# Performance work log

Hardware: AMD Instinct MI355X
Metric: run time of the kernel (lower is better)

Reference implementation:

```python
import jax, jax.numpy as jnp
import numpy as np

D_MODEL, D_Q, D_K, D_V, N = 1024, 128, 128, 128, 8192

def setup_inputs() -> dict:
    key = jax.random.key(0)
    ks = jax.random.split(key, 7)
    s = 1.0 / np.sqrt(D_MODEL)
    return {
        "x": jax.random.normal(ks[0], (N, D_MODEL), dtype=jnp.float32),
        "Wq": jax.random.uniform(ks[1], (D_MODEL, D_Q), jnp.float32, -s, s),
        "bq": jax.random.uniform(ks[2], (D_Q,), jnp.float32, -s, s),
        "Wk": jax.random.uniform(ks[3], (D_MODEL, D_K), jnp.float32, -s, s),
        "bk": jax.random.uniform(ks[4], (D_K,), jnp.float32, -s, s),
        "Wv": jax.random.uniform(ks[5], (D_MODEL, D_V), jnp.float32, -s, s),
        "bv": jax.random.uniform(ks[6], (D_V,), jnp.float32, -s, s),
    }

def reference(x, Wq, bq, Wk, bk, Wv, bv):
    q = x @ Wq + bq          # [N, d_q]
    k = x @ Wk + bk          # [N, d_k]
    v = x @ Wv + bv          # [N, d_v]
    scale = jnp.sqrt(jnp.asarray(q.shape[-1], q.dtype))
    scores = (q @ k.T) / scale          # [N, N]
    attn = jax.nn.softmax(scores, axis=1)  # matches nn.Softmax(dim=1) on 2D
    return attn @ v                     # [N, d_v]
```

## Files before the change

kernel.cpp:

```cpp
#include <hip/hip_runtime.h>


typedef __attribute__((ext_vector_type(8))) short bf16x8;
typedef __attribute__((ext_vector_type(4))) float f32x4;

#define NTOK 8192
#define DMODEL 1024
#define DH 128
#define NSPLIT 8
#define CPS 16

__device__ __forceinline__ unsigned short f2bf(float f) {
  unsigned int u = __builtin_bit_cast(unsigned int, f);
  u += 0x7fffu + ((u >> 16) & 1u);
  return (unsigned short)(u >> 16);
}

__device__ __forceinline__ unsigned int pack2bf(float a, float b) {
  return (unsigned int)f2bf(a) | ((unsigned int)f2bf(b) << 16);
}

__device__ __forceinline__ void gl2lds16(const void* gp, void* lp) {
  const __attribute__((address_space(1))) unsigned int* g =
      (const __attribute__((address_space(1))) unsigned int*)gp;
  __attribute__((address_space(3))) unsigned int* l =
      (__attribute__((address_space(3))) unsigned int*)lp;
  __builtin_amdgcn_global_load_lds(g, l, 16, 0, 0);
}

__global__ __launch_bounds__(256) void k_build_wt(const float* __restrict__ Wq,
                                                  const float* __restrict__ Wk,
                                                  const float* __restrict__ Wv,
                                                  unsigned short* __restrict__ wt) {
  __shared__ unsigned short tile[32 * 130];
  int k0 = blockIdx.x * 32;
  int p = blockIdx.y;
  int t = threadIdx.x;
  const float* W = (p == 0) ? Wq : ((p == 1) ? Wk : Wv);
  float vscale = (p == 2) ? 0.0625f : 1.0f;
#pragma unroll
  for (int i = 0; i < 16; i++) {
    int e = i * 256 + t;
    int n = e & 127, kk = e >> 7;
    tile[kk * 130 + n] = f2bf(W[(size_t)(k0 + kk) * DH + n] * vscale);
  }
  __syncthreads();
#pragma unroll
  for (int i = 0; i < 16; i++) {
    int e = i * 256 + t;
    int kk = e & 31, n = e >> 5;
    wt[(size_t)(p * DH + n) * DMODEL + k0 + kk] = tile[kk * 130 + n];
  }
}

__global__ __launch_bounds__(256, 2) void k_qkv(const float* __restrict__ x,
                                                const unsigned short* __restrict__ wt,
                                                const float* __restrict__ bq,
                                                const float* __restrict__ bk,
                                                const float* __restrict__ bv,
                                                unsigned short* __restrict__ qs,
                                                unsigned short* __restrict__ kkv,
                                                unsigned short* __restrict__ vt) {
  __shared__ float xt[2][64 * 64];
  __shared__ unsigned short wtt[2][128 * 64];
  int mt = blockIdx.x, p = blockIdx.y;
  int tid = threadIdx.x;
  int w = tid >> 6, lane = tid & 63, l16 = lane & 15, g = lane >> 4;

#define STAGE_QKV(buf, k0)                                                     \
  {                                                                            \
    _Pragma("unroll") for (int r = 0; r < 4; r++) {                            \
      int seg = r * 4 + w;                                                     \
      int xr = seg * 4 + (lane >> 4);                                          \
      int xlc = ((lane & 15) ^ (xr & 15)) & 15;                                \
      gl2lds16(&x[(size_t)(mt * 64 + xr) * DMODEL + (k0) + xlc * 4],           \
               &xt[buf][seg * 256]);                                           \
      int wc = seg * 8 + (lane >> 3);                                          \
      int wlc = ((lane & 7) ^ (wc & 7)) & 7;                                   \
      gl2lds16(&wt[(size_t)(p * DH + wc) * DMODEL + (k0) + wlc * 8],           \
               &wtt[buf][seg * 512]);                                          \
    }                                                                          \
  }

  f32x4 zero = {0.f, 0.f, 0.f, 0.f};
  f32x4 acc[8];
#pragma unroll
  for (int i = 0; i < 8; i++) acc[i] = zero;

  STAGE_QKV(0, 0);
  STAGE_QKV(1, 64);
  int arow = w * 16 + l16;
  for (int kt2 = 0; kt2 < 16; kt2++) {
    int b = kt2 & 1;
    if (kt2 < 15)
      asm volatile("s_waitcnt vmcnt(8)\n\ts_barrier" ::: "memory");
    else
      asm volatile("s_waitcnt vmcnt(0)\n\ts_barrier" ::: "memory");
    __builtin_amdgcn_sched_barrier(0);

    bf16x8 a[2];
#pragma unroll
    for (int half = 0; half < 2; half++) {
      int lc0 = half * 8 + g * 2;
      const f32x4 u0 = *(const f32x4*)&xt[b][arow * 64 + ((lc0 ^ l16) & 15) * 4];
      const f32x4 u1 = *(const f32x4*)&xt[b][arow * 64 + (((lc0 + 1) ^ l16) & 15) * 4];
      union { unsigned int u[4]; bf16x8 v; } pk;
      pk.u[0] = pack2bf(u0[0], u0[1]);
      pk.u[1] = pack2bf(u0[2], u0[3]);
      pk.u[2] = pack2bf(u1[0], u1[1]);
      pk.u[3] = pack2bf(u1[2], u1[3]);
      a[half] = pk.v;
    }
#pragma unroll
    for (int nt = 0; nt < 8; nt++) {
      int col = nt * 16 + l16;
#pragma unroll
      for (int half = 0; half < 2; half++) {
        int lc = half * 4 + g;
        bf16x8 bf = *(const bf16x8*)&wtt[b][col * 64 + ((lc ^ (col & 7)) & 7) * 8];
        acc[nt] = __builtin_amdgcn_mfma_f32_16x16x32_bf16(a[half], bf, acc[nt], 0, 0, 0);
      }
    }

    asm volatile("s_waitcnt lgkmcnt(0)\n\ts_barrier" ::: "memory");
    if (kt2 + 2 < 16) STAGE_QKV(b, (kt2 + 2) * 64);
  }
#undef STAGE_QKV

  const float* bias = (p == 0) ? bq : ((p == 1) ? bk : bv);
  float mult = (p == 0) ? (0.08838834764831845f * 1.44269504088896340f) : 1.0f;
  if (p < 2) {
    unsigned short* outp = (p == 0) ? qs : kkv;
#pragma unroll
    for (int nt = 0; nt < 8; nt++) {
      int col = nt * 16 + l16;
      float bsv = bias[col];
#pragma unroll
      for (int r = 0; r < 4; r++) {
        int row = mt * 64 + w * 16 + g * 4 + r;
        outp[(size_t)row * DH + col] = f2bf((acc[nt][r] + bsv) * mult);
      }
    }
  } else {
#pragma unroll
    for (int nt = 0; nt < 8; nt++) {
      int col = nt * 16 + l16;
      float bsv = bias[col] * 0.0625f;
      int row0 = mt * 64 + w * 16 + g * 4;
      uint2 uv;
      uv.x = pack2bf(acc[nt][0] + bsv, acc[nt][1] + bsv);
      uv.y = pack2bf(acc[nt][2] + bsv, acc[nt][3] + bsv);
      *(uint2*)(&vt[(size_t)col * NTOK + row0]) = uv;
    }
  }
}

__global__ __launch_bounds__(256, 2) void k_flash(const unsigned short* __restrict__ qs,
                                                  const unsigned short* __restrict__ kkv,
                                                  const unsigned short* __restrict__ vt,
                                                  _Float16* __restrict__ opart,
                                                  float* __restrict__ lpart) {
  __shared__ unsigned short kt[2][64 * 128];
  __shared__ unsigned short vtl[2][128 * 64];
  __shared__ unsigned short pscr[4 * 2 * 1024];
  int sp = blockIdx.x, qt = blockIdx.y;
  int tid = threadIdx.x;
  int w = tid >> 6, lane = tid & 63, l16 = lane & 15, g = lane >> 4;
  int swz2 = (l16 & 7) ^ ((l16 >> 3) << 1);

  bf16x8 qf[2][4];
  int qbase = qt * 128 + w * 32;
#pragma unroll
  for (int q2 = 0; q2 < 2; q2++)
#pragma unroll
    for (int f = 0; f < 4; f++)
      qf[q2][f] = *(const bf16x8*)(&qs[(size_t)(qbase + q2 * 16 + l16) * DH + f * 32 + g * 8]);

  int pcK[4], pcV[2], pcP[2];
#pragma unroll
  for (int f = 0; f < 4; f++) {
    int lc = f * 4 + g;
    pcK[f] = (lc & 8) | ((lc ^ l16) & 7);
  }
#pragma unroll
  for (int kb = 0; kb < 2; kb++) {
    int lc = kb * 4 + g;
    pcV[kb] = (lc ^ l16) & 7;
    pcP[kb] = (lc ^ swz2) & 7;
  }

#define STAGE_FLASH(buf, chunk)                                                 \
  {                                                                             \
    int key0 = (chunk) * 64;                                                    \
    _Pragma("unroll") for (int ii = 0; ii < 4; ii++) {                          \
      int i = w * 4 + ii;                                                       \
      int krow = 4 * i + (lane >> 4);                                           \
      int klc = ((lane & 15) & 8) | (((lane & 15) ^ krow) & 7);                 \
      gl2lds16(&kkv[(size_t)(key0 + krow) * DH + klc * 8], &kt[buf][i * 512]);  \
      int vrow = 8 * i + (lane >> 3);                                           \
      int vlc = ((lane & 7) ^ vrow) & 7;                                        \
      gl2lds16(&vt[(size_t)vrow * NTOK + key0 + vlc * 8], &vtl[buf][i * 512]);  \
    }                                                                           \
  }

  f32x4 zero = {0.f, 0.f, 0.f, 0.f};
  f32x4 o[2][8];
#pragma unroll
  for (int q2 = 0; q2 < 2; q2++)
#pragma unroll
    for (int dt = 0; dt < 8; dt++) o[q2][dt] = zero;
  float l[2] = {0.f, 0.f};

  int c0 = sp * CPS;
  STAGE_FLASH(0, c0);
  STAGE_FLASH(1, c0 + 1);

  for (int it = 0; it < CPS; it++) {
    int b = it & 1;
    if (it < CPS - 1)
      asm volatile("s_waitcnt vmcnt(8)\n\ts_barrier" ::: "memory");
    else
      asm volatile("s_waitcnt vmcnt(0)\n\ts_barrier" ::: "memory");
    __builtin_amdgcn_sched_barrier(0);

    f32x4 s[2][4];
#pragma unroll
    for (int q2 = 0; q2 < 2; q2++)
#pragma unroll
      for (int mt = 0; mt < 4; mt++) s[q2][mt] = zero;
    __builtin_amdgcn_s_setprio(1);
#pragma unroll
    for (int mt = 0; mt < 4; mt++) {
      bf16x8 kf[4];
#pragma unroll
      for (int f = 0; f < 4; f++)
        kf[f] = *(const bf16x8*)(&kt[b][(mt * 16 + l16) * 128 + pcK[f] * 8]);
#pragma unroll
      for (int f = 0; f < 4; f++) {
        s[0][mt] = __builtin_amdgcn_mfma_f32_16x16x32_bf16(kf[f], qf[0][f], s[0][mt], 0, 0, 0);
        s[1][mt] = __builtin_amdgcn_mfma_f32_16x16x32_bf16(kf[f], qf[1][f], s[1][mt], 0, 0, 0);
      }
    }
    __builtin_amdgcn_s_setprio(0);

#pragma unroll
    for (int q2 = 0; q2 < 2; q2++) {
      unsigned short* pw = &pscr[(w * 2 + q2) * 1024];
      float ssum = 0.f;
#pragma unroll
      for (int mt = 0; mt < 4; mt++) {
        float p0 = __builtin_amdgcn_exp2f(s[q2][mt][0]);
        float p1 = __builtin_amdgcn_exp2f(s[q2][mt][1]);
        float p2 = __builtin_amdgcn_exp2f(s[q2][mt][2]);
        float p3 = __builtin_amdgcn_exp2f(s[q2][mt][3]);
        ssum += (p0 + p1) + (p2 + p3);
        uint2 uv;
        uv.x = pack2bf(p0, p1);
        uv.y = pack2bf(p2, p3);
        int ch = ((mt * 2 + (g >> 1)) ^ swz2) & 7;
        *(uint2*)(&pw[l16 * 64 + ch * 8 + (g & 1) * 4]) = uv;
      }
      l[q2] += ssum;
    }

    bf16x8 pb[2][2];
#pragma unroll
    for (int q2 = 0; q2 < 2; q2++)
#pragma unroll
      for (int kb = 0; kb < 2; kb++)
        pb[q2][kb] = *(const bf16x8*)(&pscr[(w * 2 + q2) * 1024 + l16 * 64 + pcP[kb] * 8]);

    __builtin_amdgcn_s_setprio(1);
#pragma unroll
    for (int dt = 0; dt < 8; dt++)
#pragma unroll
      for (int kb = 0; kb < 2; kb++) {
        bf16x8 vf = *(const bf16x8*)(&vtl[b][(dt * 16 + l16) * 64 + pcV[kb] * 8]);
        o[0][dt] = __builtin_amdgcn_mfma_f32_16x16x32_bf16(vf, pb[0][kb], o[0][dt], 0, 0, 0);
        o[1][dt] = __builtin_amdgcn_mfma_f32_16x16x32_bf16(vf, pb[1][kb], o[1][dt], 0, 0, 0);
      }
    __builtin_amdgcn_s_setprio(0);

    asm volatile("s_waitcnt lgkmcnt(0)\n\ts_barrier" ::: "memory");
    if (it + 2 < CPS) STAGE_FLASH(b, c0 + it + 2);
  }
#undef STAGE_FLASH

#pragma unroll
  for (int q2 = 0; q2 < 2; q2++) {
    l[q2] += __shfl_xor(l[q2], 16);
    l[q2] += __shfl_xor(l[q2], 32);
    int qrow = qbase + q2 * 16 + l16;
    size_t obase = ((size_t)sp * NTOK + qrow) * DH;
#pragma unroll
    for (int dt = 0; dt < 8; dt++) {
      union { _Float16 h[4]; uint2 u; } pk;
      pk.h[0] = (_Float16)o[q2][dt][0];
      pk.h[1] = (_Float16)o[q2][dt][1];
      pk.h[2] = (_Float16)o[q2][dt][2];
      pk.h[3] = (_Float16)o[q2][dt][3];
      *(uint2*)(&opart[obase + dt * 16 + g * 4]) = pk.u;
    }
    if (g == 0) lpart[sp * NTOK + qrow] = l[q2];
  }
}

__global__ __launch_bounds__(256) void k_merge(const _Float16* __restrict__ opart,
                                               const float* __restrict__ lpart,
                                               float* __restrict__ out) {
  int gid = blockIdx.x * 256 + threadIdx.x;
  int row = gid >> 6, cp = gid & 63;
  float den = 0.f, n0 = 0.f, n1 = 0.f;
#pragma unroll
  for (int s = 0; s < NSPLIT; s++) {
    den += lpart[s * NTOK + row];
    union { unsigned int u; _Float16 h[2]; } v;
    v.u = *(const unsigned int*)&opart[((size_t)s * NTOK + row) * DH + cp * 2];
    n0 += (float)v.h[0];
    n1 += (float)v.h[1];
  }
  float inv = 16.0f / den;
  *(float2*)&out[(size_t)row * DH + cp * 2] = make_float2(n0 * inv, n1 * inv);
}

extern "C" void kernel_launch(void* const* d_in, const int* in_sizes, int n_in,
                              void* d_out, int out_size, void* d_ws, size_t ws_size,
                              hipStream_t stream) {
  const float* x  = (const float*)d_in[0];
  const float* Wq = (const float*)d_in[1];
  const float* bq = (const float*)d_in[2];
  const float* Wk = (const float*)d_in[3];
  const float* bk = (const float*)d_in[4];
  const float* Wv = (const float*)d_in[5];
  const float* bv = (const float*)d_in[6];
  float* out = (float*)d_out;

  char* ws = (char*)d_ws;
  _Float16*       opart = (_Float16*)(ws);
  unsigned short* wt  = (unsigned short*)(ws + 16777216);
  unsigned short* qsb = (unsigned short*)(ws + 17563648);
  unsigned short* kkb = (unsigned short*)(ws + 19660800);
  unsigned short* vtb = (unsigned short*)(ws + 21757952);
  float* lpart = (float*)(ws + 23855104);

  k_build_wt<<<dim3(32, 3), 256, 0, stream>>>(Wq, Wk, Wv, wt);
  k_qkv<<<dim3(128, 3), 256, 0, stream>>>(x, wt, bq, bk, bv, qsb, kkb, vtb);
  k_flash<<<dim3(NSPLIT, 64), 256, 0, stream>>>(qsb, kkb, vtb, opart, lpart);
  k_merge<<<2048, 256, 0, stream>>>(opart, lpart, out);
}
```

Measured before the change: 145.0 us.

## Software-pipeline QK^T of next chunk with softmax and PV of current chunk

Restructures the flash attention loop so the QK^T MFMA for the next key chunk is issued before the exp/pack and PV MFMAs of the current chunk, using two ping-pong score register sets and a manually unrolled loop of two. The aim is to overlap the exp2 and LDS scratch traffic with matrix-core work and hide LDS latency. Each iteration now waits with vmcnt(0) instead of vmcnt(8), which may expose more global load latency. The extra score registers raise register pressure, which could lower occupancy.

```diff
diff --git a/kernel.cpp b/kernel.cpp
--- a/kernel.cpp
+++ b/kernel.cpp
@@ -203,6 +203,62 @@
     }                                                                           \
   }
 
+#define QK_BLOCK(buf, sdst)                                                     \
+  {                                                                             \
+    _Pragma("unroll") for (int q2 = 0; q2 < 2; q2++)                            \
+      _Pragma("unroll") for (int mt = 0; mt < 4; mt++) sdst[q2][mt] = zero;     \
+    _Pragma("unroll") for (int mt = 0; mt < 4; mt++) {                          \
+      bf16x8 kf[4];                                                             \
+      _Pragma("unroll") for (int f = 0; f < 4; f++)                             \
+        kf[f] = *(const bf16x8*)(&kt[buf][(mt * 16 + l16) * 128 + pcK[f] * 8]); \
+      _Pragma("unroll") for (int f = 0; f < 4; f++) {                           \
+        sdst[0][mt] =                                                           \
+            __builtin_amdgcn_mfma_f32_16x16x32_bf16(kf[f], qf[0][f], sdst[0][mt], 0, 0, 0); \
+        sdst[1][mt] =                                                           \
+            __builtin_amdgcn_mfma_f32_16x16x32_bf16(kf[f], qf[1][f], sdst[1][mt], 0, 0, 0); \
+      }                                                                         \
+    }                                                                           \
+  }
+
+#define FITER(i, b, sprev, snext)                                               \
+  {                                                                             \
+    asm volatile("s_waitcnt vmcnt(0)\n\ts_barrier" ::: "memory");               \
+    __builtin_amdgcn_sched_barrier(0);                                          \
+    if ((i) < CPS - 1) { QK_BLOCK((b) ^ 1, snext); }                            \
+    _Pragma("unroll") for (int q2 = 0; q2 < 2; q2++) {                          \
+      unsigned short* pw = &pscr[(w * 2 + q2) * 1024];                          \
+      float ssum = 0.f;                                                         \
+      _Pragma("unroll") for (int mt = 0; mt < 4; mt++) {                        \
+        float p0 = __builtin_amdgcn_exp2f(sprev[q2][mt][0]);                    \
+        float p1 = __builtin_amdgcn_exp2f(sprev[q2][mt][1]);                    \
+        float p2 = __builtin_amdgcn_exp2f(sprev[q2][mt][2]);                    \
+        float p3 = __builtin_amdgcn_exp2f(sprev[q2][mt][3]);                    \
+        ssum += (p0 + p1) + (p2 + p3);                                          \
+        uint2 uv;                                                               \
+        uv.x = pack2bf(p0, p1);                                                 \
+        uv.y = pack2bf(p2, p3);                                                 \
+        int ch = ((mt * 2 + (g >> 1)) ^ swz2) & 7;                              \
+        *(uint2*)(&pw[l16 * 64 + ch * 8 + (g & 1) * 4]) = uv;                   \
+      }                                                                         \
+      l[q2] += ssum;                                                            \
+    }                                                                           \
+    bf16x8 pb[2][2];                                                            \
+    _Pragma("unroll") for (int q2 = 0; q2 < 2; q2++)                            \
+      _Pragma("unroll") for (int kb = 0; kb < 2; kb++)                          \
+        pb[q2][kb] =                                                            \
+            *(const bf16x8*)(&pscr[(w * 2 + q2) * 1024 + l16 * 64 + pcP[kb] * 8]); \
+    __builtin_amdgcn_s_setprio(1);                                              \
+    _Pragma("unroll") for (int dt = 0; dt < 8; dt++)                            \
+      _Pragma("unroll") for (int kb = 0; kb < 2; kb++) {                        \
+        bf16x8 vf = *(const bf16x8*)(&vtl[b][(dt * 16 + l16) * 64 + pcV[kb] * 8]); \
+        o[0][dt] = __builtin_amdgcn_mfma_f32_16x16x32_bf16(vf, pb[0][kb], o[0][dt], 0, 0, 0); \
+        o[1][dt] = __builtin_amdgcn_mfma_f32_16x16x32_bf16(vf, pb[1][kb], o[1][dt], 0, 0, 0); \
+      }                                                                         \
+    __builtin_amdgcn_s_setprio(0);                                              \
+    asm volatile("s_waitcnt lgkmcnt(0)\n\ts_barrier" ::: "memory");             \
+    if ((i) + 2 < CPS) STAGE_FLASH(b, c0 + (i) + 2);                            \
+  }
+
   f32x4 zero = {0.f, 0.f, 0.f, 0.f};
   f32x4 o[2][8];
 #pragma unroll
@@ -210,80 +266,21 @@
 #pragma unroll
     for (int dt = 0; dt < 8; dt++) o[q2][dt] = zero;
   float l[2] = {0.f, 0.f};
+  f32x4 sA[2][4], sB[2][4];
 
   int c0 = sp * CPS;
   STAGE_FLASH(0, c0);
   STAGE_FLASH(1, c0 + 1);
-
-  for (int it = 0; it < CPS; it++) {
-    int b = it & 1;
-    if (it < CPS - 1)
-      asm volatile("s_waitcnt vmcnt(8)\n\ts_barrier" ::: "memory");
-    else
-      asm volatile("s_waitcnt vmcnt(0)\n\ts_barrier" ::: "memory");
-    __builtin_amdgcn_sched_barrier(0);
-
-    f32x4 s[2][4];
-#pragma unroll
-    for (int q2 = 0; q2 < 2; q2++)
-#pragma unroll
-      for (int mt = 0; mt < 4; mt++) s[q2][mt] = zero;
-    __builtin_amdgcn_s_setprio(1);
-#pragma unroll
-    for (int mt = 0; mt < 4; mt++) {
-      bf16x8 kf[4];
-#pragma unroll
-      for (int f = 0; f < 4; f++)
-        kf[f] = *(const bf16x8*)(&kt[b][(mt * 16 + l16) * 128 + pcK[f] * 8]);
-#pragma unroll
-      for (int f = 0; f < 4; f++) {
-        s[0][mt] = __builtin_amdgcn_mfma_f32_16x16x32_bf16(kf[f], qf[0][f], s[0][mt], 0, 0, 0);
-        s[1][mt] = __builtin_amdgcn_mfma_f32_16x16x32_bf16(kf[f], qf[1][f], s[1][mt], 0, 0, 0);
-      }
-    }
-    __builtin_amdgcn_s_setprio(0);
-
-#pragma unroll
-    for (int q2 = 0; q2 < 2; q2++) {
-      unsigned short* pw = &pscr[(w * 2 + q2) * 1024];
-      float ssum = 0.f;
-#pragma unroll
-      for (int mt = 0; mt < 4; mt++) {
-        float p0 = __builtin_amdgcn_exp2f(s[q2][mt][0]);
-        float p1 = __builtin_amdgcn_exp2f(s[q2][mt][1]);
-        float p2 = __builtin_amdgcn_exp2f(s[q2][mt][2]);
-        float p3 = __builtin_amdgcn_exp2f(s[q2][mt][3]);
-        ssum += (p0 + p1) + (p2 + p3);
-        uint2 uv;
-        uv.x = pack2bf(p0, p1);
-        uv.y = pack2bf(p2, p3);
-        int ch = ((mt * 2 + (g >> 1)) ^ swz2) & 7;
-        *(uint2*)(&pw[l16 * 64 + ch * 8 + (g & 1) * 4]) = uv;
-      }
-      l[q2] += ssum;
-    }
-
-    bf16x8 pb[2][2];
-#pragma unroll
-    for (int q2 = 0; q2 < 2; q2++)
-#pragma unroll
-      for (int kb = 0; kb < 2; kb++)
-        pb[q2][kb] = *(const bf16x8*)(&pscr[(w * 2 + q2) * 1024 + l16 * 64 + pcP[kb] * 8]);
-
-    __builtin_amdgcn_s_setprio(1);
-#pragma unroll
-    for (int dt = 0; dt < 8; dt++)
-#pragma unroll
-      for (int kb = 0; kb < 2; kb++) {
-        bf16x8 vf = *(const bf16x8*)(&vtl[b][(dt * 16 + l16) * 64 + pcV[kb] * 8]);
-        o[0][dt] = __builtin_amdgcn_mfma_f32_16x16x32_bf16(vf, pb[0][kb], o[0][dt], 0, 0, 0);
-        o[1][dt] = __builtin_amdgcn_mfma_f32_16x16x32_bf16(vf, pb[1][kb], o[1][dt], 0, 0, 0);
-      }
-    __builtin_amdgcn_s_setprio(0);
-
-    asm volatile("s_waitcnt lgkmcnt(0)\n\ts_barrier" ::: "memory");
-    if (it + 2 < CPS) STAGE_FLASH(b, c0 + it + 2);
-  }
+  asm volatile("s_waitcnt vmcnt(8)\n\ts_barrier" ::: "memory");
+  __builtin_amdgcn_sched_barrier(0);
+  QK_BLOCK(0, sA);
+
+  for (int it2 = 0; it2 < CPS / 2; it2++) {
+    FITER(2 * it2, 0, sA, sB);
+    FITER(2 * it2 + 1, 1, sB, sA);
+  }
+#undef FITER
+#undef QK_BLOCK
 #undef STAGE_FLASH
 
 #pragma unroll
```

After: 170.8 us. 17.8% more time.

## Software-pipeline QK^T of next chunk ahead of PV of current chunk

Applied to the files above, without the earlier changes.

The score MFMA block for key chunk it+1 now runs right after the softmax of chunk it and before its PV MFMAs, with a prologue that computes the first chunk's scores. The aim is to let the exp/pack work and the LDS P writes overlap with independent MFMA work, so the matrix units stall less. In exchange, the wait on chunk it+1's global loads becomes a full vmcnt(0) placed mid-iteration. Each iteration still ends with an extra barrier, and the scores stay live in registers across iterations, which raises register pressure.

```diff
diff --git a/kernel.cpp b/kernel.cpp
--- a/kernel.cpp
+++ b/kernel.cpp
@@ -203,6 +203,25 @@
     }                                                                           \
   }
 
+#define QK_BLOCK(buf)                                                           \
+  {                                                                             \
+    _Pragma("unroll") for (int q2 = 0; q2 < 2; q2++)                            \
+      _Pragma("unroll") for (int mt = 0; mt < 4; mt++) s[q2][mt] = zero;        \
+    __builtin_amdgcn_s_setprio(1);                                              \
+    _Pragma("unroll") for (int mt = 0; mt < 4; mt++) {                          \
+      bf16x8 kf[4];                                                             \
+      _Pragma("unroll") for (int f = 0; f < 4; f++)                             \
+        kf[f] = *(const bf16x8*)(&kt[buf][(mt * 16 + l16) * 128 + pcK[f] * 8]); \
+      _Pragma("unroll") for (int f = 0; f < 4; f++) {                           \
+        s[0][mt] =                                                              \
+            __builtin_amdgcn_mfma_f32_16x16x32_bf16(kf[f], qf[0][f], s[0][mt], 0, 0, 0); \
+        s[1][mt] =                                                              \
+            __builtin_amdgcn_mfma_f32_16x16x32_bf16(kf[f], qf[1][f], s[1][mt], 0, 0, 0); \
+      }                                                                         \
+    }                                                                           \
+    __builtin_amdgcn_s_setprio(0);                                              \
+  }
+
   f32x4 zero = {0.f, 0.f, 0.f, 0.f};
   f32x4 o[2][8];
 #pragma unroll
@@ -210,38 +229,17 @@
 #pragma unroll
     for (int dt = 0; dt < 8; dt++) o[q2][dt] = zero;
   float l[2] = {0.f, 0.f};
+  f32x4 s[2][4];
 
   int c0 = sp * CPS;
   STAGE_FLASH(0, c0);
   STAGE_FLASH(1, c0 + 1);
+  asm volatile("s_waitcnt vmcnt(8)\n\ts_barrier" ::: "memory");
+  __builtin_amdgcn_sched_barrier(0);
+  QK_BLOCK(0);
 
   for (int it = 0; it < CPS; it++) {
     int b = it & 1;
-    if (it < CPS - 1)
-      asm volatile("s_waitcnt vmcnt(8)\n\ts_barrier" ::: "memory");
-    else
-      asm volatile("s_waitcnt vmcnt(0)\n\ts_barrier" ::: "memory");
-    __builtin_amdgcn_sched_barrier(0);
-
-    f32x4 s[2][4];
-#pragma unroll
-    for (int q2 = 0; q2 < 2; q2++)
-#pragma unroll
-      for (int mt = 0; mt < 4; mt++) s[q2][mt] = zero;
-    __builtin_amdgcn_s_setprio(1);
-#pragma unroll
-    for (int mt = 0; mt < 4; mt++) {
-      bf16x8 kf[4];
-#pragma unroll
-      for (int f = 0; f < 4; f++)
-        kf[f] = *(const bf16x8*)(&kt[b][(mt * 16 + l16) * 128 + pcK[f] * 8]);
-#pragma unroll
-      for (int f = 0; f < 4; f++) {
-        s[0][mt] = __builtin_amdgcn_mfma_f32_16x16x32_bf16(kf[f], qf[0][f], s[0][mt], 0, 0, 0);
-        s[1][mt] = __builtin_amdgcn_mfma_f32_16x16x32_bf16(kf[f], qf[1][f], s[1][mt], 0, 0, 0);
-      }
-    }
-    __builtin_amdgcn_s_setprio(0);
 
 #pragma unroll
     for (int q2 = 0; q2 < 2; q2++) {
@@ -263,6 +261,11 @@
       l[q2] += ssum;
     }
 
+    asm volatile("s_waitcnt vmcnt(0)\n\ts_barrier" ::: "memory");
+    __builtin_amdgcn_sched_barrier(0);
+
+    if (it < CPS - 1) QK_BLOCK(b ^ 1);
+
     bf16x8 pb[2][2];
 #pragma unroll
     for (int q2 = 0; q2 < 2; q2++)
@@ -284,6 +287,7 @@
     asm volatile("s_waitcnt lgkmcnt(0)\n\ts_barrier" ::: "memory");
     if (it + 2 < CPS) STAGE_FLASH(b, c0 + it + 2);
   }
+#undef QK_BLOCK
 #undef STAGE_FLASH
 
 #pragma unroll
```

Result: no change. 146.3 us (+0.9%).

## Fuse split-K merge into flash kernel via last-block atomic counter; use hardware bf16 pack

Applied to the files above, without the earlier changes.

Removes the separate merge kernel launch. Each flash block bumps a per-query-tile atomic counter, and the last of the NSPLIT blocks reduces the partial outputs and denominators into the final output. The counters are zeroed in the weight-transpose kernel. The software round-to-nearest bf16 packing is also replaced with the v_cvt_pk_bf16_f32 instruction. The merge work now runs serialized on the last-arriving block per tile, which may add tail latency in exchange for saving a launch and its gap.

```diff
diff --git a/kernel.cpp b/kernel.cpp
--- a/kernel.cpp
+++ b/kernel.cpp
@@ -16,8 +16,10 @@
   return (unsigned short)(u >> 16);
 }
 
-__device__ __forceinline__ unsigned int pack2bf(float a, float b) {
-  return (unsigned int)f2bf(a) | ((unsigned int)f2bf(b) << 16);
+__device__ __forceinline__ unsigned int cvtpk(float a, float b) {
+  unsigned int r;
+  asm("v_cvt_pk_bf16_f32 %0, %1, %2" : "=v"(r) : "v"(a), "v"(b));
+  return r;
 }
 
 __device__ __forceinline__ void gl2lds16(const void* gp, void* lp) {
@@ -31,11 +33,13 @@
 __global__ __launch_bounds__(256) void k_build_wt(const float* __restrict__ Wq,
                                                   const float* __restrict__ Wk,
                                                   const float* __restrict__ Wv,
-                                                  unsigned short* __restrict__ wt) {
+                                                  unsigned short* __restrict__ wt,
+                                                  int* __restrict__ cnt) {
   __shared__ unsigned short tile[32 * 130];
   int k0 = blockIdx.x * 32;
   int p = blockIdx.y;
   int t = threadIdx.x;
+  if (blockIdx.x == 0 && p == 0 && t < 64) cnt[t] = 0;
   const float* W = (p == 0) ? Wq : ((p == 1) ? Wk : Wv);
   float vscale = (p == 2) ? 0.0625f : 1.0f;
 #pragma unroll
@@ -105,10 +109,10 @@
       const f32x4 u0 = *(const f32x4*)&xt[b][arow * 64 + ((lc0 ^ l16) & 15) * 4];
       const f32x4 u1 = *(const f32x4*)&xt[b][arow * 64 + (((lc0 + 1) ^ l16) & 15) * 4];
       union { unsigned int u[4]; bf16x8 v; } pk;
-      pk.u[0] = pack2bf(u0[0], u0[1]);
-      pk.u[1] = pack2bf(u0[2], u0[3]);
-      pk.u[2] = pack2bf(u1[0], u1[1]);
-      pk.u[3] = pack2bf(u1[2], u1[3]);
+      pk.u[0] = cvtpk(u0[0], u0[1]);
+      pk.u[1] = cvtpk(u0[2], u0[3]);
+      pk.u[2] = cvtpk(u1[0], u1[1]);
+      pk.u[3] = cvtpk(u1[2], u1[3]);
       a[half] = pk.v;
     }
 #pragma unroll
@@ -148,8 +152,8 @@
       float bsv = bias[col] * 0.0625f;
       int row0 = mt * 64 + w * 16 + g * 4;
       uint2 uv;
-      uv.x = pack2bf(acc[nt][0] + bsv, acc[nt][1] + bsv);
-      uv.y = pack2bf(acc[nt][2] + bsv, acc[nt][3] + bsv);
+      uv.x = cvtpk(acc[nt][0] + bsv, acc[nt][1] + bsv);
+      uv.y = cvtpk(acc[nt][2] + bsv, acc[nt][3] + bsv);
       *(uint2*)(&vt[(size_t)col * NTOK + row0]) = uv;
     }
   }
@@ -159,7 +163,9 @@
                                                   const unsigned short* __restrict__ kkv,
                                                   const unsigned short* __restrict__ vt,
                                                   _Float16* __restrict__ opart,
-                                                  float* __restrict__ lpart) {
+                                                  float* __restrict__ lpart,
+                                                  float* __restrict__ out,
+                                                  int* __restrict__ cnt) {
   __shared__ unsigned short kt[2][64 * 128];
   __shared__ unsigned short vtl[2][128 * 64];
   __shared__ unsigned short pscr[4 * 2 * 1024];
@@ -255,8 +261,8 @@
         float p3 = __builtin_amdgcn_exp2f(s[q2][mt][3]);
         ssum += (p0 + p1) + (p2 + p3);
         uint2 uv;
-        uv.x = pack2bf(p0, p1);
-        uv.y = pack2bf(p2, p3);
+        uv.x = cvtpk(p0, p1);
+        uv.y = cvtpk(p2, p3);
         int ch = ((mt * 2 + (g >> 1)) ^ swz2) & 7;
         *(uint2*)(&pw[l16 * 64 + ch * 8 + (g & 1) * 4]) = uv;
       }
@@ -303,24 +309,39 @@
     }
     if (g == 0) lpart[sp * NTOK + qrow] = l[q2];
   }
-}
-
-__global__ __launch_bounds__(256) void k_merge(const _Float16* __restrict__ opart,
-                                               const float* __restrict__ lpart,
-                                               float* __restrict__ out) {
-  int gid = blockIdx.x * 256 + threadIdx.x;
-  int row = gid >> 6, cp = gid & 63;
-  float den = 0.f, n0 = 0.f, n1 = 0.f;
-#pragma unroll
-  for (int s = 0; s < NSPLIT; s++) {
-    den += lpart[s * NTOK + row];
-    union { unsigned int u; _Float16 h[2]; } v;
-    v.u = *(const unsigned int*)&opart[((size_t)s * NTOK + row) * DH + cp * 2];
-    n0 += (float)v.h[0];
-    n1 += (float)v.h[1];
-  }
-  float inv = 16.0f / den;
-  *(float2*)&out[(size_t)row * DH + cp * 2] = make_float2(n0 * inv, n1 * inv);
+
+  __threadfence();
+  int* lastp = (int*)kt;
+  float* rden = (float*)pscr;
+  if (tid == 0) *lastp = (atomicAdd(&cnt[qt], 1) == NSPLIT - 1);
+  __syncthreads();
+  if (*lastp) {
+    __threadfence();
+    if (tid < 128) {
+      int row = qt * 128 + tid;
+      float den = 0.f;
+#pragma unroll
+      for (int s2 = 0; s2 < NSPLIT; s2++) den += lpart[s2 * NTOK + row];
+      rden[tid] = 16.0f / den;
+    }
+    __syncthreads();
+#pragma unroll
+    for (int e = 0; e < 32; e++) {
+      int idx = e * 256 + tid;
+      int r = idx >> 6, cp = idx & 63;
+      int row = qt * 128 + r;
+      float n0 = 0.f, n1 = 0.f;
+#pragma unroll
+      for (int s2 = 0; s2 < NSPLIT; s2++) {
+        union { unsigned int u; _Float16 h[2]; } v;
+        v.u = *(const unsigned int*)&opart[((size_t)s2 * NTOK + row) * DH + cp * 2];
+        n0 += (float)v.h[0];
+        n1 += (float)v.h[1];
+      }
+      float inv = rden[r];
+      *(float2*)&out[(size_t)row * DH + cp * 2] = make_float2(n0 * inv, n1 * inv);
+    }
+  }
 }
 
 extern "C" void kernel_launch(void* const* d_in, const int* in_sizes, int n_in,
@@ -342,9 +363,9 @@
   unsigned short* kkb = (unsigned short*)(ws + 19660800);
   unsigned short* vtb = (unsigned short*)(ws + 21757952);
   float* lpart = (float*)(ws + 23855104);
-
-  k_build_wt<<<dim3(32, 3), 256, 0, stream>>>(Wq, Wk, Wv, wt);
+  int*   cnt   = (int*)(ws + 24117248);
+
+  k_build_wt<<<dim3(32, 3), 256, 0, stream>>>(Wq, Wk, Wv, wt, cnt);
   k_qkv<<<dim3(128, 3), 256, 0, stream>>>(x, wt, bq, bk, bv, qsb, kkb, vtb);
-  k_flash<<<dim3(NSPLIT, 64), 256, 0, stream>>>(qsb, kkb, vtb, opart, lpart);
-  k_merge<<<2048, 256, 0, stream>>>(opart, lpart, out);
-}
+  k_flash<<<dim3(NSPLIT, 64), 256, 0, stream>>>(qsb, kkb, vtb, opart, lpart, out, cnt);
+}
```

After: 225.7 us. 1.56x slower.
